# Performance work log

Hardware: AMD Instinct MI355X
Metric: run time of the kernel (lower is better)

The kernel has to match this reference:

```python
import jax, jax.numpy as jnp
import numpy as np

BETA = 0.25


def setup_inputs() -> dict:
    key = jax.random.key(0)
    k1, k2 = jax.random.split(key)
    z = jax.random.normal(k1, (16, 64, 64, 64), dtype=jnp.float32)        # [B, e_dim, H, W]
    codebook = jax.random.normal(k2, (2048, 64), dtype=jnp.float32)       # [n_e, e_dim]
    return {"z": z, "codebook": codebook}


def reference(z, codebook):
    B, C, H, W = z.shape
    n_e = codebook.shape[0]
    sg = jax.lax.stop_gradient

    zp = jnp.transpose(z, (0, 2, 3, 1))                # [B, H, W, C]
    zf = zp.reshape(-1, C)                             # [N, C]

    # nearest-code logits (inner product; CE in source is dead code)
    logits = zf @ codebook.T                           # [N, n_e]
    idx = jnp.argmax(logits, axis=1)                   # [N]

    z_q = codebook[idx].reshape(zp.shape)              # [B, H, W, C]

    # commitment + codebook loss (this overwrites the CE loss in the source)
    loss = BETA * jnp.mean((sg(z_q) - zp) ** 2) + jnp.mean((z_q - sg(zp)) ** 2)

    # straight-through estimator
    z_q_st = zp + sg(z_q - zp)

    # perplexity via one-hot mean (scatter-add instead of dense one-hot)
    counts = jnp.zeros((n_e,), dtype=zp.dtype).at[idx].add(1.0)
    e_mean = counts / idx.shape[0]
    perplexity = jnp.exp(-jnp.sum(e_mean * jnp.log(e_mean + 1e-10)))

    indices = idx.reshape(B, H * W).astype(jnp.int32)
    z_q_out = jnp.transpose(z_q_st, (0, 3, 1, 2))      # back to [B, C, H, W]
    return z_q_out, loss, perplexity, indices
```

## Files before the change

### kernel.cpp

```cpp
#include <hip/hip_runtime.h>

#define C_DIM   64
#define HW      4096
#define NROWS   65536
#define N_E     2048
#define N_ELEM  4194304
#define OUT_LOSS_OFF 4194304
#define OUT_PPL_OFF  4194305
#define OUT_IDX_OFF  4194306

#define ROWS_B   128
#define NBLOCKS  (NROWS / ROWS_B)
#define NTILE    (N_E / 16)
#define TILE_U   384

typedef __attribute__((ext_vector_type(8))) short bf16x8;
typedef __attribute__((ext_vector_type(4))) float f32x4;

__device__ __forceinline__ unsigned short f2bf(float f) {
    unsigned u = __float_as_uint(f);
    return (unsigned short)((u + 0x7FFFu + ((u >> 16) & 1u)) >> 16);
}
__device__ __forceinline__ float bf2f(unsigned short b) {
    return __uint_as_float(((unsigned)b) << 16);
}

__global__ __launch_bounds__(256) void vq_prep(
    const float* __restrict__ cb, unsigned short* __restrict__ cbp,
    int* __restrict__ counts, float* __restrict__ loss_accum,
    int* __restrict__ done)
{
    const int u = blockIdx.x * 256 + threadIdx.x;
    if (u < N_E) counts[u] = 0;
    if (u == 0)  { *loss_accum = 0.f; *done = 0; }

    const int lane = u & 63;
    const int k2   = (u >> 6) & 1;
    const int tile = u >> 7;
    const int c    = tile * 16 + (lane & 15);
    const int k0   = k2 * 32 + (lane >> 4) * 8;

    const float4 va = *(const float4*)(cb + (size_t)c * C_DIM + k0);
    const float4 vb = *(const float4*)(cb + (size_t)c * C_DIM + k0 + 4);
    const float v[8] = {va.x, va.y, va.z, va.w, vb.x, vb.y, vb.z, vb.w};

    bf16x8 s1v, s2v, s3v;
#pragma unroll
    for (int i = 0; i < 8; ++i) {
        const unsigned short s1 = f2bf(v[i]);
        const float r1 = v[i] - bf2f(s1);
        const unsigned short s2 = f2bf(r1);
        const float r2 = r1 - bf2f(s2);
        s1v[i] = (short)s1;
        s2v[i] = (short)s2;
        s3v[i] = (short)f2bf(r2);
    }
    const size_t base = ((size_t)(tile * 3 + 0) * 2 + k2) * 512 + (size_t)lane * 8;
    *(bf16x8*)(cbp + base)        = s1v;
    *(bf16x8*)(cbp + base + 1024) = s2v;
    *(bf16x8*)(cbp + base + 2048) = s3v;
}

#define M16(A_, B_, C_) __builtin_amdgcn_mfma_f32_16x16x32_bf16((A_), (B_), (C_), 0, 0, 0)

#define PASS6(AA, ACC, NT)                                                      \
    ACC = M16(AA[0], zf[0][NT][0], ACC); ACC = M16(AA[1], zf[0][NT][1], ACC);   \
    ACC = M16(AA[0], zf[1][NT][0], ACC); ACC = M16(AA[1], zf[1][NT][1], ACC);   \
    ACC = M16(AA[2], zf[0][NT][0], ACC); ACC = M16(AA[3], zf[0][NT][1], ACC);   \
    ACC = M16(AA[2], zf[1][NT][0], ACC); ACC = M16(AA[3], zf[1][NT][1], ACC);   \
    ACC = M16(AA[0], zf[2][NT][0], ACC); ACC = M16(AA[1], zf[2][NT][1], ACC);   \
    ACC = M16(AA[4], zf[0][NT][0], ACC); ACC = M16(AA[5], zf[0][NT][1], ACC);

#define COMPUTE_TILE(T_, AA)                                                    \
    {                                                                           \
        f32x4 acc0 = zero4, acc1 = zero4;                                       \
        PASS6(AA, acc0, 0)                                                      \
        PASS6(AA, acc1, 1)                                                      \
        const int cbase = (T_) * 16 + lg * 4;                                   \
        _Pragma("unroll")                                                       \
        for (int r = 0; r < 4; ++r) {                                           \
            if (acc0[r] > best0) { best0 = acc0[r]; bi0 = cbase + r; }          \
            if (acc1[r] > best1) { best1 = acc1[r]; bi1 = cbase + r; }          \
        }                                                                       \
    }

#define LOADA(AA, T_)                                                           \
    {                                                                           \
        const bf16x8* p_ = cbpf + (size_t)(T_) * TILE_U;                        \
        _Pragma("unroll")                                                       \
        for (int f = 0; f < 6; ++f) AA[f] = p_[f * 64 + lane];                  \
    }

__global__ __launch_bounds__(256, 2) void vq_mfma(
    const float* __restrict__ z, const float* __restrict__ cb,
    const unsigned short* __restrict__ cbp, float* __restrict__ out,
    int* __restrict__ counts, float* __restrict__ loss_accum,
    int* __restrict__ done)
{
    __shared__ int   sidx[ROWS_B];
    __shared__ float wsum[4];
    __shared__ int   slast;

    const int tid  = threadIdx.x;
    const int lane = tid & 63;
    const int wv   = tid >> 6;
    const int l15  = lane & 15, lg = lane >> 4;
    const int row0 = blockIdx.x * ROWS_B;
    const int b    = row0 >> 12;
    const int hw0  = row0 & 4095;
    const float* zb = z + (size_t)b * C_DIM * HW + hw0;

    if (tid == 0) slast = 0;

    bf16x8 zf[3][2][2];
#pragma unroll
    for (int nt = 0; nt < 2; ++nt) {
        const int row_l = wv * 32 + nt * 16 + l15;
#pragma unroll
        for (int k2 = 0; k2 < 2; ++k2) {
#pragma unroll
            for (int i = 0; i < 8; ++i) {
                float v = zb[(size_t)(k2 * 32 + lg * 8 + i) * HW + row_l];
                unsigned short s1 = f2bf(v);
                float r1 = v - bf2f(s1);
                unsigned short s2 = f2bf(r1);
                float r2 = r1 - bf2f(s2);
                zf[0][nt][k2][i] = (short)s1;
                zf[1][nt][k2][i] = (short)s2;
                zf[2][nt][k2][i] = (short)f2bf(r2);
            }
        }
    }

    const bf16x8* cbpf = (const bf16x8*)cbp;
    float best0 = -3.4e38f, best1 = -3.4e38f;
    int   bi0 = 0, bi1 = 0;
    const f32x4 zero4 = {0.f, 0.f, 0.f, 0.f};

    bf16x8 Acur[6], Anxt[6];
    LOADA(Acur, 0)

#pragma unroll 1
    for (int t = 0; t < NTILE; t += 2) {
        LOADA(Anxt, t + 1)
        COMPUTE_TILE(t, Acur)
        if (t + 2 < NTILE) LOADA(Acur, t + 2)
        COMPUTE_TILE(t + 1, Anxt)
    }

#pragma unroll
    for (int off = 16; off <= 32; off <<= 1) {
        float ob; int oi;
        ob = __shfl_xor(best0, off, 64); oi = __shfl_xor(bi0, off, 64);
        if (ob > best0 || (ob == best0 && oi < bi0)) { best0 = ob; bi0 = oi; }
        ob = __shfl_xor(best1, off, 64); oi = __shfl_xor(bi1, off, 64);
        if (ob > best1 || (ob == best1 && oi < bi1)) { best1 = ob; bi1 = oi; }
    }
    if (lane < 32) {
        const int nt = lane >> 4;
        const int row_l = wv * 32 + lane;
        const int ii = (nt == 0) ? bi0 : bi1;
        sidx[row_l] = ii;
        out[OUT_IDX_OFF + row0 + row_l] = (float)ii;
        atomicAdd(&counts[ii], 1);
    }
    __syncthreads();

    float* ob0 = out + (size_t)b * C_DIM * HW + hw0;
    float lsum = 0.f;
#pragma unroll
    for (int j = 0; j < 8; ++j) {
        const int m = j * 256 + tid;
        const int r = m & 127, c4 = m >> 7;
        const float4 q4 = *(const float4*)(cb + (size_t)sidx[r] * C_DIM + c4 * 4);
#pragma unroll
        for (int q = 0; q < 4; ++q) {
            const int c = c4 * 4 + q;
            const float zv = zb[(size_t)c * HW + r];
            const float qv = (q == 0) ? q4.x : (q == 1) ? q4.y : (q == 2) ? q4.z : q4.w;
            const float d = qv - zv;
            lsum += d * d;
            ob0[(size_t)c * HW + r] = zv + d;
        }
    }
    for (int off = 32; off > 0; off >>= 1) lsum += __shfl_down(lsum, off, 64);
    if (lane == 0) wsum[wv] = lsum;
    __syncthreads();

    if (tid == 0) {
        atomicAdd(loss_accum, wsum[0] + wsum[1] + wsum[2] + wsum[3]);
        __threadfence();
        const int tk = atomicAdd(done, 1);
        if (tk == NBLOCKS - 1) slast = 1;
    }
    __syncthreads();
    if (slast) {
        __threadfence();
        float h = 0.f;
        for (int e = tid; e < N_E; e += 256) {
            const int cnt = atomicAdd(&counts[e], 0);
            const float em = (float)cnt * (1.0f / (float)NROWS);
            h -= em * logf(em + 1e-10f);
        }
        for (int off = 32; off > 0; off >>= 1) h += __shfl_down(h, off, 64);
        if (lane == 0) wsum[wv] = h;
        __syncthreads();
        if (tid == 0) {
            const float H = wsum[0] + wsum[1] + wsum[2] + wsum[3];
            const float L = atomicAdd(loss_accum, 0.f);
            const float m = L * (1.0f / (float)N_ELEM);
            out[OUT_LOSS_OFF] = 0.25f * m + m;
            out[OUT_PPL_OFF]  = expf(H);
        }
    }
}

extern "C" void kernel_launch(void* const* d_in, const int* in_sizes, int n_in,
                              void* d_out, int out_size, void* d_ws, size_t ws_size,
                              hipStream_t stream)
{
    const float* z  = (const float*)d_in[0];
    const float* cb = (const float*)d_in[1];
    float* out = (float*)d_out;

    int*            counts     = (int*)d_ws;
    float*          loss_accum = (float*)((char*)d_ws + N_E * sizeof(int));
    int*            done       = (int*)((char*)d_ws + N_E * sizeof(int) + 4);
    unsigned short* cbp        = (unsigned short*)((char*)d_ws + 16384);

    vq_prep<<<64, 256, 0, stream>>>(cb, cbp, counts, loss_accum, done);
    vq_mfma<<<NBLOCKS, 256, 0, stream>>>(z, cb, cbp, out, counts, loss_accum, done);
}
```

Measured before the change: 168.4 us.

## Stage codebook tiles into LDS via global_load_lds double buffering

Replaces the per-wave register prefetch of the split-bf16 codebook from global memory with a block-cooperative double-buffered staging into shared memory using direct global-to-LDS loads. All four waves then read the same tile from LDS, which removes the redundant global/L2 traffic where each wave fetched the whole codebook itself. The cost is a __syncthreads per tile (128 barriers per block), extra LDS use that may affect occupancy, and the loss of the register-level prefetch overlap.

```diff
diff --git a/kernel.cpp b/kernel.cpp
--- a/kernel.cpp
+++ b/kernel.cpp
@@ -12,7 +12,7 @@
 #define ROWS_B   128
 #define NBLOCKS  (NROWS / ROWS_B)
 #define NTILE    (N_E / 16)
-#define TILE_U   384
+#define TILE_B   6144
 
 typedef __attribute__((ext_vector_type(8))) short bf16x8;
 typedef __attribute__((ext_vector_type(4))) float f32x4;
@@ -84,11 +84,14 @@
         }                                                                       \
     }
 
-#define LOADA(AA, T_)                                                           \
-    {                                                                           \
-        const bf16x8* p_ = cbpf + (size_t)(T_) * TILE_U;                        \
-        _Pragma("unroll")                                                       \
-        for (int f = 0; f < 6; ++f) AA[f] = p_[f * 64 + lane];                  \
+typedef const __attribute__((address_space(1))) unsigned int* gas_ptr;
+typedef __attribute__((address_space(3))) unsigned int* las_ptr;
+#define STAGE(BUF, T_)                                                          \
+    for (int c = wv; c < 6; c += 4) {                                           \
+        __builtin_amdgcn_global_load_lds(                                       \
+            (gas_ptr)((const char*)cbp + (size_t)(T_) * TILE_B + c * 1024       \
+                      + lane * 16),                                             \
+            (las_ptr)((char*)&lbuf[BUF][0] + c * 1024), 16, 0, 0);              \
     }
 
 __global__ __launch_bounds__(256, 2) void vq_mfma(
@@ -97,6 +100,7 @@
     int* __restrict__ counts, float* __restrict__ loss_accum,
     int* __restrict__ done)
 {
+    __shared__ __align__(16) unsigned short lbuf[2][TILE_B / 2];
     __shared__ int   sidx[ROWS_B];
     __shared__ float wsum[4];
     __shared__ int   slast;
@@ -111,6 +115,8 @@
     const float* zb = z + (size_t)b * C_DIM * HW + hw0;
 
     if (tid == 0) slast = 0;
+
+    STAGE(0, 0)
 
     bf16x8 zf[3][2][2];
 #pragma unroll
@@ -131,21 +137,24 @@
             }
         }
     }
-
-    const bf16x8* cbpf = (const bf16x8*)cbp;
+    __syncthreads();
+
     float best0 = -3.4e38f, best1 = -3.4e38f;
     int   bi0 = 0, bi1 = 0;
     const f32x4 zero4 = {0.f, 0.f, 0.f, 0.f};
 
-    bf16x8 Acur[6], Anxt[6];
-    LOADA(Acur, 0)
-
 #pragma unroll 1
-    for (int t = 0; t < NTILE; t += 2) {
-        LOADA(Anxt, t + 1)
-        COMPUTE_TILE(t, Acur)
-        if (t + 2 < NTILE) LOADA(Acur, t + 2)
-        COMPUTE_TILE(t + 1, Anxt)
+    for (int t = 0; t < NTILE; ++t) {
+        if (t + 1 < NTILE) STAGE((t + 1) & 1, t + 1)
+
+        const bf16x8* Ab = (const bf16x8*)&lbuf[t & 1][0];
+        bf16x8 A[6];
+#pragma unroll
+        for (int f = 0; f < 6; ++f) A[f] = Ab[f * 64 + lane];
+
+        COMPUTE_TILE(t, A)
+
+        __syncthreads();
     }
 
 #pragma unroll
```

Result: slower. 196.2 us (+16.5%).
